# Optimization experiments

Hardware: AMD Instinct MI355X
Metric: run time of the kernel (lower is better)

Reference implementation:

```python
import jax, jax.numpy as jnp
import numpy as np

N, IN_F, OUT_F, H = 2048, 512, 256, 4
NH = OUT_F // H  # n_hidden per head (is_concat=True)
NEG_SLOPE = 0.2
NEG_INF = -1e9  # finite stand-in for -inf in masked softmax


def setup_inputs() -> dict:
    key = jax.random.key(0)
    k1, k2, k3, k4, k5 = jax.random.split(key, 5)
    h = jax.random.normal(k1, (N, IN_F), dtype=jnp.float32)
    adj = jax.random.randint(k2, (N, N), 0, 2).astype(jnp.float32)
    adj = jnp.maximum(adj, jnp.eye(N, dtype=jnp.float32))  # self-loops -> no empty rows
    adj_mat = adj[:, :, None]  # [N, N, 1]
    s = jax.random.uniform(k3, (N, N, 1), dtype=jnp.float32)
    W_lin = jax.random.normal(k4, (IN_F, H * NH), dtype=jnp.float32) / np.sqrt(IN_F)
    attn_w = jax.random.normal(k5, (2 * NH,), dtype=jnp.float32) / np.sqrt(2 * NH)
    return {"h": h, "adj_mat": adj_mat, "s": s, "W_lin": W_lin, "attn_w": attn_w}


def reference(h, adj_mat, s, W_lin, attn_w):
    n = h.shape[0]
    g = (h @ W_lin).reshape(n, H, NH)  # [N, H, nh]
    # attn(Linear(2*nh,1)) on cat(g_i, g_j) == a_src.g_i + a_dst.g_j
    a_src, a_dst = attn_w[:NH], attn_w[NH:]
    el = jnp.einsum('nhf,f->nh', g, a_src)  # source (row i) term
    er = jnp.einsum('nhf,f->nh', g, a_dst)  # dest   (col j) term
    e = jax.nn.leaky_relu(el[:, None, :] + er[None, :, :], NEG_SLOPE)  # [N, N, H]
    mask = adj_mat == 0  # [N, N, 1] broadcasts over heads
    e = jnp.where(mask, NEG_INF, e)
    s_m = jnp.where(mask, NEG_INF, s)  # [N, N, 1]
    a = jax.nn.softmax(e, axis=1)
    s_prime = jax.nn.softmax(s_m, axis=1)
    new_attention = jax.nn.softmax(a + s_prime, axis=1)  # [N, N, H] (dropout=identity, eval)
    attn_res = jnp.einsum('ijh,jhf->ihf', new_attention, g)  # [N, H, nh]
    return attn_res.reshape(n, H * NH)
```

## Files before the change

### kernel.cpp

```cpp
#include <hip/hip_runtime.h>

#define NN 2048
#define KK 512

typedef __attribute__((ext_vector_type(8))) short bf16x8;
typedef __attribute__((ext_vector_type(4))) float f32x4;

__device__ inline ushort f2bf(float x) {
  union { float f; unsigned u; } v; v.f = x;
  unsigned r = v.u + 0x7fffu + ((v.u >> 16) & 1u);
  return (ushort)(r >> 16);
}

__global__ __launch_bounds__(256) void k_wprep(
    const float* __restrict__ W, ushort* __restrict__ wthi,
    ushort* __restrict__ wtlo) {
  __shared__ float ts[64][65];
  const int t = threadIdx.x;
  const int kb = (blockIdx.x >> 2) * 64;
  const int nb = (blockIdx.x & 3) * 64;
  const int r = t >> 6, c = t & 63;
#pragma unroll
  for (int p = 0; p < 16; ++p)
    ts[p * 4 + r][c] = W[(size_t)(kb + p * 4 + r) * 256 + nb + c];
  __syncthreads();
#pragma unroll
  for (int p = 0; p < 16; ++p) {
    int n = p * 4 + r;
    int k = c;
    float v = ts[k][n];
    union { float f; unsigned u; } q; q.f = v;
    ushort hi = (ushort)(q.u >> 16);
    union { float f; unsigned u; } hf; hf.u = q.u & 0xffff0000u;
    ushort lo = f2bf(v - hf.f);
    size_t off = (size_t)(nb + n) * KK + kb + k;
    wthi[off] = hi;
    wtlo[off] = lo;
  }
}

__global__ __launch_bounds__(256) void k_gemm(
    const float* __restrict__ hin, const ushort* __restrict__ wthi,
    const ushort* __restrict__ wtlo, const float* __restrict__ aw,
    ushort* __restrict__ gTb,
    float* __restrict__ Eel, float* __restrict__ Fel,
    float* __restrict__ Eer_jh, float* __restrict__ Fer_jh,
    float* __restrict__ Eer_hj, float* __restrict__ Fer_hj) {
  __shared__ float hs[16][516];
  const int tid = threadIdx.x;
  const int i0 = blockIdx.x * 16;
#pragma unroll
  for (int p = 0; p < 8; ++p) {
    int g4 = tid + p * 256;
    int row = g4 >> 7, col = (g4 & 127) << 2;
    *(float4*)&hs[row][col] = *(const float4*)(hin + (size_t)(i0 + row) * KK + col);
  }
  __syncthreads();

  const int h = tid >> 6;
  const int lane = tid & 63;
  const int il = lane & 15;
  const int kg = lane >> 4;

  f32x4 acc[4];
#pragma unroll
  for (int nt = 0; nt < 4; ++nt) acc[nt] = (f32x4){0.f, 0.f, 0.f, 0.f};

  const ushort* bh_base = wthi + (size_t)(h * 64 + il) * KK;
  const ushort* bl_base = wtlo + (size_t)(h * 64 + il) * KK;

#pragma unroll 4
  for (int ks = 0; ks < 16; ++ks) {
    const int ko = ks * 32 + kg * 8;
    float4 a01 = *(const float4*)&hs[il][ko];
    float4 a23 = *(const float4*)&hs[il][ko + 4];
    float av[8] = {a01.x, a01.y, a01.z, a01.w, a23.x, a23.y, a23.z, a23.w};
    union { unsigned u[4]; bf16x8 v; } Ah, Al;
#pragma unroll
    for (int p = 0; p < 4; ++p) {
      union { float f; unsigned u; } u0, u1;
      u0.f = av[2 * p]; u1.f = av[2 * p + 1];
      Ah.u[p] = (u0.u >> 16) | (u1.u & 0xffff0000u);
      union { float f; unsigned u; } h0, h1;
      h0.u = u0.u & 0xffff0000u;
      h1.u = u1.u & 0xffff0000u;
      union { float f; unsigned u; } r0, r1;
      r0.f = av[2 * p] - h0.f;
      r1.f = av[2 * p + 1] - h1.f;
      Al.u[p] = (r0.u >> 16) | (r1.u & 0xffff0000u);
    }
#pragma unroll
    for (int nt = 0; nt < 4; ++nt) {
      bf16x8 Bh = *(const bf16x8*)(bh_base + nt * 16 * KK + ko);
      bf16x8 Bl = *(const bf16x8*)(bl_base + nt * 16 * KK + ko);
      acc[nt] = __builtin_amdgcn_mfma_f32_16x16x32_bf16(Ah.v, Bh, acc[nt], 0, 0, 0);
      acc[nt] = __builtin_amdgcn_mfma_f32_16x16x32_bf16(Al.v, Bh, acc[nt], 0, 0, 0);
      acc[nt] = __builtin_amdgcn_mfma_f32_16x16x32_bf16(Ah.v, Bl, acc[nt], 0, 0, 0);
    }
  }

  const int jb = (i0 >> 3) + (kg >> 1);
  const int halfoff = (kg & 1) * 4;
#pragma unroll
  for (int nt = 0; nt < 4; ++nt) {
    const int f = h * 64 + nt * 16 + il;
    unsigned w0 = (unsigned)f2bf(acc[nt][0]) | ((unsigned)f2bf(acc[nt][1]) << 16);
    unsigned w1 = (unsigned)f2bf(acc[nt][2]) | ((unsigned)f2bf(acc[nt][3]) << 16);
    uint2 pk = make_uint2(w0, w1);
    *(uint2*)(gTb + (size_t)jb * 2048 + f * 8 + halfoff) = pk;
  }

  float ela[4] = {0.f, 0.f, 0.f, 0.f}, era[4] = {0.f, 0.f, 0.f, 0.f};
#pragma unroll
  for (int nt = 0; nt < 4; ++nt) {
    float as = aw[nt * 16 + il];
    float ad = aw[64 + nt * 16 + il];
#pragma unroll
    for (int q = 0; q < 4; ++q) {
      ela[q] += acc[nt][q] * as;
      era[q] += acc[nt][q] * ad;
    }
  }
#pragma unroll
  for (int m = 1; m < 16; m <<= 1) {
#pragma unroll
    for (int q = 0; q < 4; ++q) {
      ela[q] += __shfl_xor(ela[q], m);
      era[q] += __shfl_xor(era[q], m);
    }
  }
  if (il == 0) {
#pragma unroll
    for (int q = 0; q < 4; ++q) {
      const int row = i0 + kg * 4 + q;
      float eel = __expf(ela[q]);
      float fel = __expf(0.2f * ela[q]);
      float eer = __expf(era[q]);
      float fer = __expf(0.2f * era[q]);
      Eel[row * 4 + h] = eel;
      Fel[row * 4 + h] = fel;
      Eer_jh[row * 4 + h] = eer;
      Fer_jh[row * 4 + h] = fer;
      Eer_hj[h * NN + row] = eer;
      Fer_hj[h * NN + row] = fer;
    }
  }
}

__global__ __launch_bounds__(256) void k_rowz(
    const float* __restrict__ adj, const float* __restrict__ s,
    const float* __restrict__ Eel, const float* __restrict__ Fel,
    const float* __restrict__ Eer_jh, const float* __restrict__ Fer_jh,
    float* __restrict__ rZ1, float* __restrict__ rZ2,
    unsigned long long* __restrict__ maskb) {
  const int row = blockIdx.x;
  const int tid = threadIdx.x;
  const int wq = tid >> 6;
  const int lane = tid & 63;

  float4 e4 = *(const float4*)(Eel + row * 4);
  float4 f4 = *(const float4*)(Fel + row * 4);
  const float eel[4] = {e4.x, e4.y, e4.z, e4.w};
  const float fel[4] = {f4.x, f4.y, f4.z, f4.w};

  float z1[4] = {0.f, 0.f, 0.f, 0.f};
  float z2 = 0.f;

  const float* ap = adj + (size_t)row * NN + wq * 512;
  const float* sp = s + (size_t)row * NN + wq * 512;

#pragma unroll
  for (int it = 0; it < 8; ++it) {
    const int j = it * 64 + lane;
    float a = ap[j];
    float sv = sp[j];
    bool nb = (a != 0.f);
    unsigned long long m = __ballot(nb);
    if (lane == 0) maskb[row * 32 + wq * 8 + it] = m;
    const int jg = wq * 512 + j;
    float4 eer4 = *(const float4*)(Eer_jh + jg * 4);
    float4 fer4 = *(const float4*)(Fer_jh + jg * 4);
    z2 += nb ? __expf(sv) : 0.f;
    float ev[4] = {eer4.x, eer4.y, eer4.z, eer4.w};
    float fv[4] = {fer4.x, fer4.y, fer4.z, fer4.w};
#pragma unroll
    for (int h = 0; h < 4; ++h) {
      float p = eel[h] * ev[h];
      float q = fel[h] * fv[h];
      float E = fmaxf(p, q);
      z1[h] += nb ? E : 0.f;
    }
  }

#pragma unroll
  for (int m = 1; m < 64; m <<= 1) {
    z2 += __shfl_xor(z2, m);
#pragma unroll
    for (int h = 0; h < 4; ++h) z1[h] += __shfl_xor(z1[h], m);
  }

  __shared__ float wr[4][5];
  if (lane == 0) {
    wr[wq][0] = z1[0]; wr[wq][1] = z1[1]; wr[wq][2] = z1[2]; wr[wq][3] = z1[3];
    wr[wq][4] = z2;
  }
  __syncthreads();
  if (tid < 5) {
    float sum = wr[0][tid] + wr[1][tid] + wr[2][tid] + wr[3][tid];
    if (tid < 4) rZ1[row * 4 + tid] = 1.f / sum;
    else rZ2[row] = 1.f / sum;
  }
}

__global__ __launch_bounds__(256, 8) void k_attn(
    const float* __restrict__ s, const unsigned long long* __restrict__ maskb,
    const ushort* __restrict__ gTb,
    const float* __restrict__ Eel, const float* __restrict__ Fel,
    const float* __restrict__ Eer_hj, const float* __restrict__ Fer_hj,
    const float* __restrict__ rZ1, const float* __restrict__ rZ2,
    _Float16* __restrict__ U, float* __restrict__ Z3p) {
  __shared__ float esb_s[16][132];
  __shared__ float eer_s[4][132];
  __shared__ float fer_s[4][132];

  const int tid = threadIdx.x;
  const int h = tid >> 6;
  const int lane = tid & 63;
  const int il = lane & 15;
  const int kg = lane >> 4;
  const int ib = blockIdx.x >> 4;
  const int jc = blockIdx.x & 15;
  const int i0 = ib * 16;
  const int jb0 = jc * 128;
  const int row = i0 + il;

  {
    const int r = tid >> 4;
    const int c8 = (tid & 15) * 8;
    const int rowr = i0 + r;
    const float rz2r = rZ2[rowr];
    unsigned long long mw = maskb[rowr * 32 + jc * 2 + (c8 >> 6)];
    unsigned byte_ = (unsigned)(mw >> (c8 & 63)) & 0xffu;
    float4 sa = *(const float4*)(s + (size_t)rowr * NN + jb0 + c8);
    float4 sb = *(const float4*)(s + (size_t)rowr * NN + jb0 + c8 + 4);
    float sv[8] = {sa.x, sa.y, sa.z, sa.w, sb.x, sb.y, sb.z, sb.w};
#pragma unroll
    for (int e = 0; e < 8; ++e)
      esb_s[r][c8 + e] = ((byte_ >> e) & 1u) ? __expf(sv[e]) * rz2r : 0.f;
  }
  {
    const int hh = (tid & 127) >> 5;
    const int c4 = (tid & 31) * 4;
    const float* src = (tid < 128) ? Eer_hj : Fer_hj;
    float4 v = *(const float4*)(src + hh * NN + jb0 + c4);
    float* dst = (tid < 128) ? &eer_s[hh][c4] : &fer_s[hh][c4];
    dst[0] = v.x; dst[1] = v.y; dst[2] = v.z; dst[3] = v.w;
  }
  __syncthreads();

  const float rz1 = rZ1[row * 4 + h];
  const float eelz = Eel[row * 4 + h] * rz1;
  const float felz = Fel[row * 4 + h] * rz1;

  const unsigned long long* mp = maskb + row * 32 + jc * 2;
  const unsigned long long m0 = mp[0];
  const unsigned long long m1 = mp[1];

  f32x4 acc[4];
#pragma unroll
  for (int nt = 0; nt < 4; ++nt) acc[nt] = (f32x4){0.f, 0.f, 0.f, 0.f};
  float z3 = 0.f;

  const ushort* bp = gTb + (size_t)(jc * 16 + kg) * 2048 + (h * 64 + il) * 8;

#pragma unroll
  for (int ks = 0; ks < 4; ++ks) {
    const ushort* bks = bp + (size_t)(ks * 4) * 2048;
    bf16x8 B0 = *(const bf16x8*)(bks);
    bf16x8 B1 = *(const bf16x8*)(bks + 128);
    bf16x8 B2 = *(const bf16x8*)(bks + 256);
    bf16x8 B3 = *(const bf16x8*)(bks + 384);

    unsigned long long w = (ks & 2) ? m1 : m0;
    unsigned byte_ = (unsigned)(w >> ((ks & 1) * 32 + kg * 8)) & 0xffu;
    const int jl = ks * 32 + kg * 8;

    bf16x8 A;
#pragma unroll
    for (int e = 0; e < 8; ++e) {
      bool nb = (byte_ >> e) & 1u;
      float p = eelz * eer_s[h][jl + e];
      float q = felz * fer_s[h][jl + e];
      float tt = nb ? (fmaxf(p, q) + esb_s[il][jl + e]) : 0.f;
      float c = __expf(tt);
      z3 += c;
      A[e] = (short)f2bf(c);
    }

    acc[0] = __builtin_amdgcn_mfma_f32_16x16x32_bf16(A, B0, acc[0], 0, 0, 0);
    acc[1] = __builtin_amdgcn_mfma_f32_16x16x32_bf16(A, B1, acc[1], 0, 0, 0);
    acc[2] = __builtin_amdgcn_mfma_f32_16x16x32_bf16(A, B2, acc[2], 0, 0, 0);
    acc[3] = __builtin_amdgcn_mfma_f32_16x16x32_bf16(A, B3, acc[3], 0, 0, 0);
  }

  z3 += __shfl_xor(z3, 16);
  z3 += __shfl_xor(z3, 32);
  if (lane < 16)
    Z3p[jc * (NN * 4) + (i0 + lane) * 4 + h] = z3;

  _Float16* up = U + (size_t)jc * (NN * 256) + (size_t)i0 * 256 + h * 64 + il;
#pragma unroll
  for (int nt = 0; nt < 4; ++nt)
#pragma unroll
    for (int q = 0; q < 4; ++q)
      up[(size_t)(kg * 4 + q) * 256 + nt * 16] = (_Float16)acc[nt][q];
}

__global__ __launch_bounds__(256) void k_final(
    const _Float16* __restrict__ U, const float* __restrict__ Z3p,
    float* __restrict__ out) {
  const int i = blockIdx.x;
  const int c = threadIdx.x;
  const int h = c >> 6;
  float u = 0.f, z = 0.f;
#pragma unroll
  for (int p = 0; p < 16; ++p) {
    u += (float)U[(size_t)p * (NN * 256) + (size_t)i * 256 + c];
    z += Z3p[p * (NN * 4) + i * 4 + h];
  }
  out[(size_t)i * 256 + c] = u / z;
}

extern "C" void kernel_launch(void* const* d_in, const int* in_sizes, int n_in,
                              void* d_out, int out_size, void* d_ws, size_t ws_size,
                              hipStream_t stream) {
  const float* hin = (const float*)d_in[0];
  const float* adj = (const float*)d_in[1];
  const float* s = (const float*)d_in[2];
  const float* W = (const float*)d_in[3];
  const float* aw = (const float*)d_in[4];
  float* out = (float*)d_out;

  float* ws = (float*)d_ws;
  float* Eel    = ws;
  float* Fel    = ws + 8192;
  float* Eer_jh = ws + 16384;
  float* Fer_jh = ws + 24576;
  float* Eer_hj = ws + 32768;
  float* Fer_hj = ws + 40960;
  float* rZ1    = ws + 49152;
  float* rZ2    = ws + 57344;
  float* Z3p    = ws + 59392;
  unsigned long long* maskb = (unsigned long long*)(ws + 190464);
  ushort* wthi  = (ushort*)(ws + 321536);
  ushort* wtlo  = (ushort*)(ws + 387072);
  ushort* gTb   = (ushort*)(ws + 452608);
  _Float16* U   = (_Float16*)(ws + 714752);

  k_wprep<<<32, 256, 0, stream>>>(W, wthi, wtlo);
  k_gemm<<<128, 256, 0, stream>>>(hin, wthi, wtlo, aw, gTb, Eel, Fel, Eer_jh, Fer_jh, Eer_hj, Fer_hj);
  k_rowz<<<2048, 256, 0, stream>>>(adj, s, Eel, Fel, Eer_jh, Fer_jh, rZ1, rZ2, maskb);
  k_attn<<<2048, 256, 0, stream>>>(s, maskb, gTb, Eel, Fel, Eer_hj, Fer_hj, rZ1, rZ2, U, Z3p);
  k_final<<<2048, 256, 0, stream>>>(U, Z3p, out);
}
```

Measured before the change: 73.79 us.

## Fuse row normalizers, attention aggregation and final reduce into one kernel

Replaces the row-sum, attention and final-reduction kernels with a single kernel in which each 512-thread block owns 8 rows. It computes masks, exp(s) and softmax normalizers into shared memory, then runs the MFMA aggregation over all columns and divides in-block. This removes the large fp16 partial-result buffer, the partial-sum buffer and two launches. In exchange the grid shrinks to 256 blocks with long per-wave loops, and half of each 16-row MFMA tile duplicates rows.

```diff
diff --git a/kernel.cpp b/kernel.cpp
--- a/kernel.cpp
+++ b/kernel.cpp
@@ -147,151 +147,110 @@
   }
 }
 
-__global__ __launch_bounds__(256) void k_rowz(
+__global__ __launch_bounds__(512, 2) void k_mega(
     const float* __restrict__ adj, const float* __restrict__ s,
+    const ushort* __restrict__ gTb,
     const float* __restrict__ Eel, const float* __restrict__ Fel,
     const float* __restrict__ Eer_jh, const float* __restrict__ Fer_jh,
-    float* __restrict__ rZ1, float* __restrict__ rZ2,
-    unsigned long long* __restrict__ maskb) {
-  const int row = blockIdx.x;
+    const float* __restrict__ Eer_hj, const float* __restrict__ Fer_hj,
+    float* __restrict__ out) {
+  __shared__ float es_s[8][2052];
+  __shared__ unsigned long long maskl[8][34];
+  __shared__ float zrow[8][8];
+  __shared__ float z3L[2][4][8];
+  __shared__ float dacc[2][4][8][64];
+
   const int tid = threadIdx.x;
-  const int wq = tid >> 6;
+  const int w = tid >> 6;
   const int lane = tid & 63;
-
-  float4 e4 = *(const float4*)(Eel + row * 4);
-  float4 f4 = *(const float4*)(Fel + row * 4);
-  const float eel[4] = {e4.x, e4.y, e4.z, e4.w};
-  const float fel[4] = {f4.x, f4.y, f4.z, f4.w};
-
-  float z1[4] = {0.f, 0.f, 0.f, 0.f};
-  float z2 = 0.f;
-
-  const float* ap = adj + (size_t)row * NN + wq * 512;
-  const float* sp = s + (size_t)row * NN + wq * 512;
-
-#pragma unroll
-  for (int it = 0; it < 8; ++it) {
-    const int j = it * 64 + lane;
-    float a = ap[j];
-    float sv = sp[j];
-    bool nb = (a != 0.f);
-    unsigned long long m = __ballot(nb);
-    if (lane == 0) maskb[row * 32 + wq * 8 + it] = m;
-    const int jg = wq * 512 + j;
-    float4 eer4 = *(const float4*)(Eer_jh + jg * 4);
-    float4 fer4 = *(const float4*)(Fer_jh + jg * 4);
-    z2 += nb ? __expf(sv) : 0.f;
-    float ev[4] = {eer4.x, eer4.y, eer4.z, eer4.w};
-    float fv[4] = {fer4.x, fer4.y, fer4.z, fer4.w};
-#pragma unroll
-    for (int h = 0; h < 4; ++h) {
-      float p = eel[h] * ev[h];
-      float q = fel[h] * fv[h];
-      float E = fmaxf(p, q);
-      z1[h] += nb ? E : 0.f;
-    }
-  }
-
-#pragma unroll
-  for (int m = 1; m < 64; m <<= 1) {
-    z2 += __shfl_xor(z2, m);
-#pragma unroll
-    for (int h = 0; h < 4; ++h) z1[h] += __shfl_xor(z1[h], m);
-  }
-
-  __shared__ float wr[4][5];
-  if (lane == 0) {
-    wr[wq][0] = z1[0]; wr[wq][1] = z1[1]; wr[wq][2] = z1[2]; wr[wq][3] = z1[3];
-    wr[wq][4] = z2;
+  const int i0 = blockIdx.x * 8;
+
+  {
+    const int row = i0 + w;
+    const float* ap = adj + (size_t)row * NN;
+    const float* sp = s + (size_t)row * NN;
+    float4 e4 = *(const float4*)(Eel + row * 4);
+    float4 f4 = *(const float4*)(Fel + row * 4);
+    const float eel[4] = {e4.x, e4.y, e4.z, e4.w};
+    const float fel[4] = {f4.x, f4.y, f4.z, f4.w};
+    float z1[4] = {0.f, 0.f, 0.f, 0.f};
+    float z2 = 0.f;
+#pragma unroll 4
+    for (int it = 0; it < 32; ++it) {
+      const int j = it * 64 + lane;
+      float a = ap[j];
+      float sv = sp[j];
+      bool nb = (a != 0.f);
+      unsigned long long m = __ballot(nb);
+      if (lane == 0) maskl[w][it] = m;
+      float es = nb ? __expf(sv) : 0.f;
+      es_s[w][j] = es;
+      z2 += es;
+      float4 eer4 = *(const float4*)(Eer_jh + j * 4);
+      float4 fer4 = *(const float4*)(Fer_jh + j * 4);
+      float ev[4] = {eer4.x, eer4.y, eer4.z, eer4.w};
+      float fv[4] = {fer4.x, fer4.y, fer4.z, fer4.w};
+#pragma unroll
+      for (int h = 0; h < 4; ++h) {
+        float E = fmaxf(eel[h] * ev[h], fel[h] * fv[h]);
+        z1[h] += nb ? E : 0.f;
+      }
+    }
+#pragma unroll
+    for (int m = 1; m < 64; m <<= 1) {
+      z2 += __shfl_xor(z2, m);
+#pragma unroll
+      for (int h = 0; h < 4; ++h) z1[h] += __shfl_xor(z1[h], m);
+    }
+    if (lane == 0) {
+#pragma unroll
+      for (int h = 0; h < 4; ++h) zrow[w][h] = 1.f / z1[h];
+      zrow[w][4] = 1.f / z2;
+    }
   }
   __syncthreads();
-  if (tid < 5) {
-    float sum = wr[0][tid] + wr[1][tid] + wr[2][tid] + wr[3][tid];
-    if (tid < 4) rZ1[row * 4 + tid] = 1.f / sum;
-    else rZ2[row] = 1.f / sum;
-  }
-}
-
-__global__ __launch_bounds__(256, 8) void k_attn(
-    const float* __restrict__ s, const unsigned long long* __restrict__ maskb,
-    const ushort* __restrict__ gTb,
-    const float* __restrict__ Eel, const float* __restrict__ Fel,
-    const float* __restrict__ Eer_hj, const float* __restrict__ Fer_hj,
-    const float* __restrict__ rZ1, const float* __restrict__ rZ2,
-    _Float16* __restrict__ U, float* __restrict__ Z3p) {
-  __shared__ float esb_s[16][132];
-  __shared__ float eer_s[4][132];
-  __shared__ float fer_s[4][132];
-
-  const int tid = threadIdx.x;
-  const int h = tid >> 6;
-  const int lane = tid & 63;
+
+  const int h = w & 3;
+  const int jh = w >> 2;
   const int il = lane & 15;
   const int kg = lane >> 4;
-  const int ib = blockIdx.x >> 4;
-  const int jc = blockIdx.x & 15;
-  const int i0 = ib * 16;
-  const int jb0 = jc * 128;
-  const int row = i0 + il;
-
-  {
-    const int r = tid >> 4;
-    const int c8 = (tid & 15) * 8;
-    const int rowr = i0 + r;
-    const float rz2r = rZ2[rowr];
-    unsigned long long mw = maskb[rowr * 32 + jc * 2 + (c8 >> 6)];
-    unsigned byte_ = (unsigned)(mw >> (c8 & 63)) & 0xffu;
-    float4 sa = *(const float4*)(s + (size_t)rowr * NN + jb0 + c8);
-    float4 sb = *(const float4*)(s + (size_t)rowr * NN + jb0 + c8 + 4);
-    float sv[8] = {sa.x, sa.y, sa.z, sa.w, sb.x, sb.y, sb.z, sb.w};
-#pragma unroll
-    for (int e = 0; e < 8; ++e)
-      esb_s[r][c8 + e] = ((byte_ >> e) & 1u) ? __expf(sv[e]) * rz2r : 0.f;
-  }
-  {
-    const int hh = (tid & 127) >> 5;
-    const int c4 = (tid & 31) * 4;
-    const float* src = (tid < 128) ? Eer_hj : Fer_hj;
-    float4 v = *(const float4*)(src + hh * NN + jb0 + c4);
-    float* dst = (tid < 128) ? &eer_s[hh][c4] : &fer_s[hh][c4];
-    dst[0] = v.x; dst[1] = v.y; dst[2] = v.z; dst[3] = v.w;
-  }
-  __syncthreads();
-
-  const float rz1 = rZ1[row * 4 + h];
+  const int r = il & 7;
+  const int row = i0 + r;
+
+  const float rz1 = zrow[r][h];
+  const float rz2 = zrow[r][4];
   const float eelz = Eel[row * 4 + h] * rz1;
   const float felz = Fel[row * 4 + h] * rz1;
 
-  const unsigned long long* mp = maskb + row * 32 + jc * 2;
-  const unsigned long long m0 = mp[0];
-  const unsigned long long m1 = mp[1];
-
   f32x4 acc[4];
 #pragma unroll
   for (int nt = 0; nt < 4; ++nt) acc[nt] = (f32x4){0.f, 0.f, 0.f, 0.f};
   float z3 = 0.f;
 
-  const ushort* bp = gTb + (size_t)(jc * 16 + kg) * 2048 + (h * 64 + il) * 8;
-
-#pragma unroll
-  for (int ks = 0; ks < 4; ++ks) {
+  const ushort* bp = gTb + (size_t)(jh * 128 + kg) * 2048 + (h * 64 + il) * 8;
+  const float* eerp = Eer_hj + h * NN + jh * 1024 + kg * 8;
+  const float* ferp = Fer_hj + h * NN + jh * 1024 + kg * 8;
+
+#pragma unroll 4
+  for (int ks = 0; ks < 32; ++ks) {
     const ushort* bks = bp + (size_t)(ks * 4) * 2048;
     bf16x8 B0 = *(const bf16x8*)(bks);
     bf16x8 B1 = *(const bf16x8*)(bks + 128);
     bf16x8 B2 = *(const bf16x8*)(bks + 256);
     bf16x8 B3 = *(const bf16x8*)(bks + 384);
 
-    unsigned long long w = (ks & 2) ? m1 : m0;
-    unsigned byte_ = (unsigned)(w >> ((ks & 1) * 32 + kg * 8)) & 0xffu;
-    const int jl = ks * 32 + kg * 8;
+    unsigned long long mw = maskl[r][jh * 16 + (ks >> 1)];
+    unsigned byte_ = (unsigned)(mw >> ((ks & 1) * 32 + kg * 8)) & 0xffu;
+    const int jl = jh * 1024 + ks * 32 + kg * 8;
+    const int go = ks * 32;
 
     bf16x8 A;
 #pragma unroll
     for (int e = 0; e < 8; ++e) {
       bool nb = (byte_ >> e) & 1u;
-      float p = eelz * eer_s[h][jl + e];
-      float q = felz * fer_s[h][jl + e];
-      float tt = nb ? (fmaxf(p, q) + esb_s[il][jl + e]) : 0.f;
+      float p = eelz * eerp[go + e];
+      float q = felz * ferp[go + e];
+      float tt = nb ? (fmaxf(p, q) + es_s[r][jl + e] * rz2) : 0.f;
       float c = __expf(tt);
       z3 += c;
       A[e] = (short)f2bf(c);
@@ -305,30 +264,28 @@
 
   z3 += __shfl_xor(z3, 16);
   z3 += __shfl_xor(z3, 32);
-  if (lane < 16)
-    Z3p[jc * (NN * 4) + (i0 + lane) * 4 + h] = z3;
-
-  _Float16* up = U + (size_t)jc * (NN * 256) + (size_t)i0 * 256 + h * 64 + il;
-#pragma unroll
-  for (int nt = 0; nt < 4; ++nt)
-#pragma unroll
-    for (int q = 0; q < 4; ++q)
-      up[(size_t)(kg * 4 + q) * 256 + nt * 16] = (_Float16)acc[nt][q];
-}
-
-__global__ __launch_bounds__(256) void k_final(
-    const _Float16* __restrict__ U, const float* __restrict__ Z3p,
-    float* __restrict__ out) {
-  const int i = blockIdx.x;
-  const int c = threadIdx.x;
-  const int h = c >> 6;
-  float u = 0.f, z = 0.f;
-#pragma unroll
-  for (int p = 0; p < 16; ++p) {
-    u += (float)U[(size_t)p * (NN * 256) + (size_t)i * 256 + c];
-    z += Z3p[p * (NN * 4) + i * 4 + h];
-  }
-  out[(size_t)i * 256 + c] = u / z;
+  if (lane < 8) z3L[jh][h][lane] = z3;
+
+  if (kg < 2) {
+#pragma unroll
+    for (int nt = 0; nt < 4; ++nt)
+#pragma unroll
+      for (int q = 0; q < 4; ++q)
+        dacc[jh][h][kg * 4 + q][nt * 16 + il] = acc[nt][q];
+  }
+  __syncthreads();
+
+#pragma unroll
+  for (int p = 0; p < 4; ++p) {
+    const int v = tid + p * 512;
+    const int rr = v >> 8;
+    const int c = v & 255;
+    const int hh = c >> 6;
+    const int f = c & 63;
+    float u = dacc[0][hh][rr][f] + dacc[1][hh][rr][f];
+    float z = z3L[0][hh][rr] + z3L[1][hh][rr];
+    out[(size_t)(i0 + rr) * 256 + c] = u / z;
+  }
 }
 
 extern "C" void kernel_launch(void* const* d_in, const int* in_sizes, int n_in,
@@ -348,18 +305,11 @@
   float* Fer_jh = ws + 24576;
   float* Eer_hj = ws + 32768;
   float* Fer_hj = ws + 40960;
-  float* rZ1    = ws + 49152;
-  float* rZ2    = ws + 57344;
-  float* Z3p    = ws + 59392;
-  unsigned long long* maskb = (unsigned long long*)(ws + 190464);
-  ushort* wthi  = (ushort*)(ws + 321536);
-  ushort* wtlo  = (ushort*)(ws + 387072);
-  ushort* gTb   = (ushort*)(ws + 452608);
-  _Float16* U   = (_Float16*)(ws + 714752);
+  ushort* wthi  = (ushort*)(ws + 49152);
+  ushort* wtlo  = (ushort*)(ws + 114688);
+  ushort* gTb   = (ushort*)(ws + 180224);
 
   k_wprep<<<32, 256, 0, stream>>>(W, wthi, wtlo);
   k_gemm<<<128, 256, 0, stream>>>(hin, wthi, wtlo, aw, gTb, Eel, Fel, Eer_jh, Fer_jh, Eer_hj, Fer_hj);
-  k_rowz<<<2048, 256, 0, stream>>>(adj, s, Eel, Fel, Eer_jh, Fer_jh, rZ1, rZ2, maskb);
-  k_attn<<<2048, 256, 0, stream>>>(s, maskb, gTb, Eel, Fel, Eer_hj, Fer_hj, rZ1, rZ2, U, Z3p);
-  k_final<<<2048, 256, 0, stream>>>(U, Z3p, out);
-}
+  k_mega<<<256, 512, 0, stream>>>(adj, s, gTb, Eel, Fel, Eer_jh, Fer_jh, Eer_hj, Fer_hj, out);
+}
```

Result: slower. 88.94 us (+20.5%).
